# Optimization experiments

Hardware: AMD Instinct MI355X
Metric: run time of the kernel (lower is better)

## Reference

```python
import jax, jax.numpy as jnp
import numpy as np
import math

T_SCALE = 99
FEAT_DIM = 400
BATCH = 2
C = 256
NH = 8
NS = 32
NSPB = 3
RATIO = 0.5
LOCAL_STEP = 33


def build_sample_mask(T=T_SCALE, ns=NS, nspb=NSPB, ratio=RATIO):
    # Vectorized port of _get_interp1d_mask. Flat layout: [time, (bin, start, end)].
    N = ns * nspb
    e_idx, s_idx = np.meshgrid(np.arange(T), np.arange(T), indexing='ij')
    valid = s_idx < e_idx
    starts_i = s_idx[valid].astype(np.int64)
    ends_i = e_idx[valid].astype(np.int64)
    starts = starts_i.astype(np.float64)
    ends = ends_i.astype(np.float64)
    center = ends - starts + 1.0
    xmin = starts - center * ratio
    plen = (ends + center * ratio) - xmin
    S = xmin[:, None] + (plen / (N - 1.0))[:, None] * np.arange(N)[None, :]  # [P, N]
    down = np.trunc(S).astype(np.int64)  # matches int(math.modf(s)[1]) (trunc toward 0)
    dec = S - down                       # can be negative when s < 0, as in the original
    up = np.ceil(S).astype(np.int64)
    bin_col = (np.arange(N) // nspb)[None, :] * (T * T) + (starts_i * T + ends_i)[:, None]
    M = np.zeros(T * ns * T * T, np.float64)
    vd = (down >= 0) & (down <= T - 1)
    np.add.at(M, (down * (ns * T * T) + bin_col)[vd], ((1.0 - dec) / nspb)[vd])
    vu = (up >= 0) & (up <= T - 1)
    np.add.at(M, (up * (ns * T * T) + bin_col)[vu], (dec / nspb)[vu])
    return M.reshape(T, ns * T * T).astype(np.float32)


def pos_ebb(scale, size):
    pos = jnp.arange(scale, dtype=jnp.float32)[:, None]
    div = jnp.exp(jnp.arange(0, size, 2, dtype=jnp.float32) * (-math.log(10000.0) / size))
    ang = pos * div
    # interleave sin (even) / cos (odd)
    return jnp.stack([jnp.sin(ang), jnp.cos(ang)], axis=-1).reshape(scale, size)


def layer_norm(x, g, b, eps=1e-5):
    mu = jnp.mean(x, -1, keepdims=True)
    var = jnp.mean((x - mu) ** 2, -1, keepdims=True)
    return (x - mu) * jax.lax.rsqrt(var + eps) * g + b


def mha(x, w_qkv, b_qkv, w_o, b_o, nh=NH):
    t, b, c = x.shape
    hd = c // nh
    q, k, v = jnp.split(x @ w_qkv.T + b_qkv, 3, axis=-1)
    q = q.reshape(t, b, nh, hd)
    k = k.reshape(t, b, nh, hd)
    v = v.reshape(t, b, nh, hd)
    att = jnp.einsum('qbhd,kbhd->bhqk', q, k) / math.sqrt(hd)
    att = jax.nn.softmax(att, axis=-1)
    o = jnp.einsum('bhqk,kbhd->qbhd', att, v).reshape(t, b, c)
    return o @ w_o.T + b_o


def encoder(x, p):
    # PyTorch post-norm TransformerEncoder (eval mode, dropout off) + final LayerNorm
    (qkv_w, qkv_b, o_w, o_b, l1_w, l1_b, l2_w, l2_b, n1_g, n1_b, n2_g, n2_b, nf_g, nf_b) = p
    for i in range(qkv_w.shape[0]):
        a = mha(x, qkv_w[i], qkv_b[i], o_w[i], o_b[i])
        x = layer_norm(x + a, n1_g[i], n1_b[i])
        f = jax.nn.relu(x @ l1_w[i].T + l1_b[i]) @ l2_w[i].T + l2_b[i]
        x = layer_norm(x + f, n2_g[i], n2_b[i])
    return layer_norm(x, nf_g, nf_b)


def conv1d(x, w, b, pad, groups=1):
    y = jax.lax.conv_general_dilated(x, w, (1,), [(pad, pad)],
                                     dimension_numbers=('NCH', 'OIH', 'NCH'),
                                     feature_group_count=groups)
    return y + b[None, :, None]


def conv2d(x, w, b, pad):
    y = jax.lax.conv_general_dilated(x, w, (1, 1), [(pad, pad), (pad, pad)],
                                     dimension_numbers=('NCHW', 'OIHW', 'NCHW'))
    return y + b[None, :, None, None]


def conv3d(x, w, b, stride):
    y = jax.lax.conv_general_dilated(x, w, stride, [(0, 0)] * 3,
                                     dimension_numbers=('NCDHW', 'OIDHW', 'NCDHW'))
    return y + b[None, :, None, None, None]


def _forward(x, cb_w, cb_b, tg_qkv_w, tg_qkv_b, tg_o_w, tg_o_b, tg_l1_w, tg_l1_b, tg_l2_w, tg_l2_b, tg_n1_g, tg_n1_b, tg_n2_g, tg_n2_b, tg_nf_g, tg_nf_b, tl_qkv_w, tl_qkv_b, tl_o_w, tl_o_b, tl_l1_w, tl_l1_b, tl_l2_w, tl_l2_b, tl_n1_g, tl_n1_b, tl_n2_g, tl_n2_b, tl_nf_g, tl_nf_b, s1_w, s1_b, s2_w, s2_b, c3_w, c3_b, p1_w, p1_b, p2_w, p2_b, p3_w, p3_b, sample_mask):
    B, _, T = x.shape
    base = jax.nn.relu(conv1d(x, cb_w, cb_b, pad=1, groups=4))  # [B,C,T]
    # local transformer on LOCAL_STEP-strided windows
    group = T // LOCAL_STEP
    tl_p = (tl_qkv_w, tl_qkv_b, tl_o_w, tl_o_b, tl_l1_w, tl_l1_b, tl_l2_w, tl_l2_b, tl_n1_g, tl_n1_b, tl_n2_g, tl_n2_b, tl_nf_g, tl_nf_b)
    feat = base.reshape(B, C, LOCAL_STEP, group).transpose(2, 3, 0, 1).reshape(LOCAL_STEP, B * group, C)
    feat = encoder(feat + pos_ebb(LOCAL_STEP, C)[:, None, :], tl_p)
    local = feat.reshape(LOCAL_STEP * group, B, C).transpose(1, 2, 0)  # [B,C,T]
    # global bidirectional transformer (shared weights, flipped second pass)
    tg_p = (tg_qkv_w, tg_qkv_b, tg_o_w, tg_o_b, tg_l1_w, tg_l1_b, tg_l2_w, tg_l2_b, tg_n1_g, tg_n1_b, tg_n2_g, tg_n2_b, tg_nf_g, tg_nf_b)
    g = base.transpose(2, 0, 1)  # [T,B,C]
    pe = pos_ebb(T, C)[:, None, :]
    f1 = encoder(g + pe, tg_p)
    f2 = encoder(g[::-1] + pe, tg_p)
    base2 = local + (f1 + f2[::-1]).transpose(1, 2, 0)  # [B,C,T]
    s = jax.nn.relu(conv1d(base2, s1_w, s1_b, pad=1, groups=4))
    start1 = jax.nn.sigmoid(conv1d(s, s2_w, s2_b, pad=0))[:, 0, :]  # [B,T]
    # boundary-matching layer: dense matmul against precomputed interp mask
    bm = jnp.matmul(base2, sample_mask).reshape(B, C, NS, T, T)
    p = jax.nn.relu(conv3d(bm, c3_w, c3_b, (NS, 1, 1)))[:, :, 0]  # [B,C,T,T]
    p = jax.nn.relu(conv2d(p, p1_w, p1_b, pad=1))
    p = jax.nn.relu(conv2d(p, p2_w, p2_b, pad=1))
    cm = jax.nn.sigmoid(conv2d(p, p3_w, p3_b, pad=0))  # [B,2,T,T]
    return cm, start1


def setup_inputs() -> dict:
    key = jax.random.key(0)
    ks = iter(jax.random.split(key, 80))
    def rnd(shape):
        return 0.02 * jax.random.normal(next(ks), shape, dtype=jnp.float32)
    inp = {'x': jax.random.normal(next(ks), (BATCH, FEAT_DIM, T_SCALE), dtype=jnp.float32)}
    inp['cb_w'] = rnd((C, FEAT_DIM // 4, 3)); inp['cb_b'] = jnp.zeros((C,), jnp.float32)
    for pre, n in (('tg', 6), ('tl', 3)):
        inp[pre + '_qkv_w'] = rnd((n, 3 * C, C)); inp[pre + '_qkv_b'] = jnp.zeros((n, 3 * C), jnp.float32)
        inp[pre + '_o_w'] = rnd((n, C, C)); inp[pre + '_o_b'] = jnp.zeros((n, C), jnp.float32)
        inp[pre + '_l1_w'] = rnd((n, 1024, C)); inp[pre + '_l1_b'] = jnp.zeros((n, 1024), jnp.float32)
        inp[pre + '_l2_w'] = rnd((n, C, 1024)); inp[pre + '_l2_b'] = jnp.zeros((n, C), jnp.float32)
        inp[pre + '_n1_g'] = jnp.ones((n, C), jnp.float32); inp[pre + '_n1_b'] = jnp.zeros((n, C), jnp.float32)
        inp[pre + '_n2_g'] = jnp.ones((n, C), jnp.float32); inp[pre + '_n2_b'] = jnp.zeros((n, C), jnp.float32)
        inp[pre + '_nf_g'] = jnp.ones((C,), jnp.float32); inp[pre + '_nf_b'] = jnp.zeros((C,), jnp.float32)
    inp['s1_w'] = rnd((C, C // 4, 3)); inp['s1_b'] = jnp.zeros((C,), jnp.float32)
    inp['s2_w'] = rnd((1, C, 1)); inp['s2_b'] = jnp.zeros((1,), jnp.float32)
    inp['c3_w'] = rnd((C, C, NS, 1, 1)); inp['c3_b'] = jnp.zeros((C,), jnp.float32)
    inp['p1_w'] = rnd((C, C, 3, 3)); inp['p1_b'] = jnp.zeros((C,), jnp.float32)
    inp['p2_w'] = rnd((C, C, 3, 3)); inp['p2_b'] = jnp.zeros((C,), jnp.float32)
    inp['p3_w'] = rnd((2, C, 1, 1)); inp['p3_b'] = jnp.zeros((2,), jnp.float32)
    inp['sample_mask'] = jnp.asarray(build_sample_mask())  # [T, NS*T*T], exact BMN interp mask
    return inp


def reference(x, cb_w, cb_b, tg_qkv_w, tg_qkv_b, tg_o_w, tg_o_b, tg_l1_w, tg_l1_b, tg_l2_w, tg_l2_b, tg_n1_g, tg_n1_b, tg_n2_g, tg_n2_b, tg_nf_g, tg_nf_b, tl_qkv_w, tl_qkv_b, tl_o_w, tl_o_b, tl_l1_w, tl_l1_b, tl_l2_w, tl_l2_b, tl_n1_g, tl_n1_b, tl_n2_g, tl_n2_b, tl_nf_g, tl_nf_b, s1_w, s1_b, s2_w, s2_b, c3_w, c3_b, p1_w, p1_b, p2_w, p2_b, p3_w, p3_b, sample_mask):
    return _forward(x, cb_w, cb_b, tg_qkv_w, tg_qkv_b, tg_o_w, tg_o_b, tg_l1_w, tg_l1_b, tg_l2_w, tg_l2_b, tg_n1_g, tg_n1_b, tg_n2_g, tg_n2_b, tg_nf_g, tg_nf_b, tl_qkv_w, tl_qkv_b, tl_o_w, tl_o_b, tl_l1_w, tl_l1_b, tl_l2_w, tl_l2_b, tl_n1_g, tl_n1_b, tl_n2_g, tl_n2_b, tl_nf_g, tl_nf_b, s1_w, s1_b, s2_w, s2_b, c3_w, c3_b, p1_w, p1_b, p2_w, p2_b, p3_w, p3_b, sample_mask)
```

## Files before the change

kernel.cpp:

```cpp
#include <hip/hip_runtime.h>
#include <math.h>

#define T99   99
#define CC    256
#define NHH   8
#define FEAT  400
#define NS_   32
#define LSTEP 33

typedef __attribute__((ext_vector_type(8))) short s8v;
typedef __attribute__((ext_vector_type(4))) float f4v;

__device__ __forceinline__ void mfma_bf16(f4v& d, s8v a, s8v b) {
  asm volatile("v_mfma_f32_16x16x32_bf16 %0, %1, %2, %0" : "+v"(d) : "v"(a), "v"(b));
}

__device__ __forceinline__ unsigned short f2bf(float f) {
  union { float f; unsigned u; } x; x.f = f;
  unsigned r = x.u + 0x7FFFu + ((x.u >> 16) & 1u);
  return (unsigned short)(r >> 16);
}
__device__ __forceinline__ float bf2f(unsigned short h) {
  union { unsigned u; float f; } x; x.u = ((unsigned)h) << 16;
  return x.f;
}
__device__ __forceinline__ float blo(unsigned u) { union { unsigned x; float f; } c; c.x = u << 16; return c.f; }
__device__ __forceinline__ float bhi(unsigned u) { union { unsigned x; float f; } c; c.x = u & 0xffff0000u; return c.f; }

__device__ __forceinline__ float pe_val(int pos, int c) {
  int i = c >> 1;
  float freq = expf((float)(2 * i) * (-0.03597789207803197f));
  float ang = (float)pos * freq;
  return (c & 1) ? cosf(ang) : sinf(ang);
}

__global__ __launch_bounds__(128) void k_convbase(const float* __restrict__ x,
                                                  const float* __restrict__ w,
                                                  const float* __restrict__ bias,
                                                  float* __restrict__ base) {
  int b = blockIdx.x >> 8, co = blockIdx.x & 255, t = threadIdx.x;
  if (t >= T99) return;
  int g = co >> 6;
  float acc = bias[co];
  const float* xp = x + (size_t)(b * FEAT + g * 100) * T99;
  const float* wp = w + (size_t)co * 300;
  for (int ic = 0; ic < 100; ++ic) {
    float x0 = (t > 0)  ? xp[ic * T99 + t - 1] : 0.f;
    float x1 = xp[ic * T99 + t];
    float x2 = (t < 98) ? xp[ic * T99 + t + 1] : 0.f;
    acc += wp[ic * 3] * x0 + wp[ic * 3 + 1] * x1 + wp[ic * 3 + 2] * x2;
  }
  base[(size_t)(b * CC + co) * T99 + t] = fmaxf(acc, 0.f);
}

__global__ __launch_bounds__(256) void k_convW(const float* __restrict__ qkv, const float* __restrict__ o,
                                               const float* __restrict__ l1, const float* __restrict__ l2,
                                               int L, unsigned short* __restrict__ dst) {
  int total = L * 786432;
  for (int idx = blockIdx.x * 256 + threadIdx.x; idx < total; idx += gridDim.x * 256) {
    int l = idx / 786432, r = idx % 786432;
    float v;
    if (r < 196608)      v = qkv[(size_t)l * 196608 + r];
    else if (r < 262144) v = o[(size_t)l * 65536 + (r - 196608)];
    else if (r < 524288) v = l1[(size_t)l * 262144 + (r - 262144)];
    else                 v = l2[(size_t)l * 262144 + (r - 524288)];
    dst[idx] = f2bf(v);
  }
}

__global__ __launch_bounds__(256) void k_build_xg(const float* __restrict__ base, float* __restrict__ xg,
                                                  unsigned short* __restrict__ xgb) {
  int idx = blockIdx.x * 256 + threadIdx.x;
  int t = idx >> 10, r = idx & 1023, b4 = r >> 8, c = r & 255;
  float v = (b4 < 2) ? base[(size_t)(b4 * CC + c) * T99 + t]
                     : base[(size_t)((b4 - 2) * CC + c) * T99 + (98 - t)];
  v += pe_val(t, c);
  xg[idx] = v; xgb[idx] = f2bf(v);
}

__global__ __launch_bounds__(256) void k_build_xl(const float* __restrict__ base, float* __restrict__ xl,
                                                  unsigned short* __restrict__ xlb) {
  int idx = blockIdx.x * 256 + threadIdx.x;
  int ls = idx / 1536, r = idx % 1536, j = r >> 8, c = r & 255;
  int g = j >> 1, b = j & 1, t = ls * 3 + g;
  float v = base[(size_t)(b * CC + c) * T99 + t] + pe_val(ls, c);
  xl[idx] = v; xlb[idx] = f2bf(v);
}

__device__ __forceinline__ void gemm_body(const unsigned short* __restrict__ A,
                                          const unsigned short* __restrict__ W,
                                          const float* __restrict__ bias,
                                          const float* __restrict__ R,
                                          float* __restrict__ Y,
                                          unsigned short* __restrict__ Yb,
                                          int M, int N, int K, int flags,
                                          int m0, int n0) {
  __shared__ __align__(16) unsigned short Al[64][40];
  __shared__ __align__(16) unsigned short Bl[64][40];
  int tid = threadIdx.x;
  int lane = tid & 63, w = tid >> 6, wm = w >> 1, wn = w & 1;
  int sp = tid >> 2, kc = (tid & 3) << 3;
  f4v zero4 = {0.f, 0.f, 0.f, 0.f};
  f4v acc[2][2];
#pragma unroll
  for (int mt = 0; mt < 2; ++mt)
#pragma unroll
    for (int nt = 0; nt < 2; ++nt) acc[mt][nt] = zero4;

  for (int k0 = 0; k0 < K; k0 += 32) {
    s8v av = {0, 0, 0, 0, 0, 0, 0, 0};
    int row = m0 + sp;
    if (row < M) av = *(const s8v*)&A[(size_t)row * K + k0 + kc];
    *(s8v*)&Al[sp][kc] = av;
    *(s8v*)&Bl[sp][kc] = *(const s8v*)&W[(size_t)(n0 + sp) * K + k0 + kc];
    __syncthreads();
    s8v af[2], bf[2];
#pragma unroll
    for (int mt = 0; mt < 2; ++mt)
      af[mt] = *(const s8v*)&Al[wm * 32 + mt * 16 + (lane & 15)][(lane >> 4) * 8];
#pragma unroll
    for (int nt = 0; nt < 2; ++nt)
      bf[nt] = *(const s8v*)&Bl[wn * 32 + nt * 16 + (lane & 15)][(lane >> 4) * 8];
#pragma unroll
    for (int mt = 0; mt < 2; ++mt)
#pragma unroll
      for (int nt = 0; nt < 2; ++nt) mfma_bf16(acc[mt][nt], af[mt], bf[nt]);
    __syncthreads();
  }
  asm volatile("s_nop 7\n\ts_nop 7\n\ts_nop 4");
#pragma unroll
  for (int mt = 0; mt < 2; ++mt) {
#pragma unroll
    for (int nt = 0; nt < 2; ++nt) {
      int col = n0 + wn * 32 + nt * 16 + (lane & 15);
      float bv = bias[col];
#pragma unroll
      for (int r = 0; r < 2 * 2; ++r) {
        int row = m0 + wm * 32 + mt * 16 + (lane >> 4) * 4 + r;
        if (row < M) {
          float v = acc[mt][nt][r] + bv;
          if (flags & 2) v += R[(size_t)row * N + col];
          if (flags & 1) v = fmaxf(v, 0.f);
          if (!(flags & 8)) Y[(size_t)row * N + col] = v;
          if (flags & 4) Yb[(size_t)row * N + col] = f2bf(v);
        }
      }
    }
  }
}

__global__ __launch_bounds__(256) void k_gemmb(const unsigned short* __restrict__ A,
                                               const unsigned short* __restrict__ W,
                                               const float* __restrict__ bias,
                                               const float* __restrict__ R,
                                               float* __restrict__ Y,
                                               unsigned short* __restrict__ Yb,
                                               int M, int N, int K, int flags) {
  gemm_body(A, W, bias, R, Y, Yb, M, N, K, flags, blockIdx.x * 64, blockIdx.y * 64);
}

__global__ __launch_bounds__(256) void k_gemmb2(const unsigned short* __restrict__ A0,
                                                const unsigned short* __restrict__ W0,
                                                const float* __restrict__ bias0,
                                                const float* __restrict__ R0,
                                                float* __restrict__ Y0,
                                                unsigned short* __restrict__ Yb0,
                                                int M0,
                                                const unsigned short* __restrict__ A1,
                                                const unsigned short* __restrict__ W1,
                                                const float* __restrict__ bias1,
                                                const float* __restrict__ R1,
                                                float* __restrict__ Y1,
                                                unsigned short* __restrict__ Yb1,
                                                int M1,
                                                int N, int K, int flags) {
  int m0 = blockIdx.x * 64;
  if (blockIdx.z == 0) {
    if (m0 >= M0) return;
    gemm_body(A0, W0, bias0, R0, Y0, Yb0, M0, N, K, flags, m0, blockIdx.y * 64);
  } else {
    if (m0 >= M1) return;
    gemm_body(A1, W1, bias1, R1, Y1, Yb1, M1, N, K, flags, m0, blockIdx.y * 64);
  }
}

__device__ __forceinline__ void attn_body(const unsigned short* __restrict__ qkv,
                                          unsigned short* __restrict__ attb,
                                          int T_, int B_, int bid) {
  __shared__ float qv[32];
  __shared__ float red[128];
  __shared__ float pv[128];
  int tid = threadIdx.x;
  int q = bid % T_;
  int h = (bid / T_) % NHH;
  int b = bid / (T_ * NHH);
  if (tid < 32) qv[tid] = bf2f(qkv[(size_t)(q * B_ + b) * 768 + h * 32 + tid]);
  __syncthreads();
  float s = -1e30f;
  if (tid < T_) {
    const unsigned short* kp = qkv + (size_t)(tid * B_ + b) * 768 + 256 + h * 32;
    float d = 0;
#pragma unroll
    for (int i = 0; i < 32; ++i) d += qv[i] * bf2f(kp[i]);
    s = d * 0.176776695296636881f;
  }
  red[tid] = s; __syncthreads();
  for (int o = 64; o > 0; o >>= 1) { if (tid < o) red[tid] = fmaxf(red[tid], red[tid + o]); __syncthreads(); }
  float mx = red[0]; __syncthreads();
  float p = (tid < T_) ? expf(s - mx) : 0.f;
  pv[tid] = p; red[tid] = p; __syncthreads();
  for (int o = 64; o > 0; o >>= 1) { if (tid < o) red[tid] += red[tid + o]; __syncthreads(); }
  float denom = red[0];
  if (tid < 32) {
    float o = 0;
    for (int k = 0; k < T_; ++k) o += pv[k] * bf2f(qkv[(size_t)(k * B_ + b) * 768 + 512 + h * 32 + tid]);
    attb[(size_t)(q * B_ + b) * 256 + h * 32 + tid] = f2bf(o / denom);
  }
}

__global__ __launch_bounds__(128) void k_attn(const unsigned short* __restrict__ qkv,
                                              unsigned short* __restrict__ attb,
                                              int T_, int B_) {
  attn_body(qkv, attb, T_, B_, blockIdx.x);
}

__global__ __launch_bounds__(128) void k_attn2(const unsigned short* __restrict__ qkv0,
                                               unsigned short* __restrict__ attb0, int T0, int B0,
                                               const unsigned short* __restrict__ qkv1,
                                               unsigned short* __restrict__ attb1, int T1, int B1) {
  int bid = blockIdx.x;
  if (blockIdx.z == 0) {
    if (bid >= B0 * NHH * T0) return;
    attn_body(qkv0, attb0, T0, B0, bid);
  } else {
    if (bid >= B1 * NHH * T1) return;
    attn_body(qkv1, attb1, T1, B1, bid);
  }
}

__device__ __forceinline__ void ln_body(const float* __restrict__ X, const float* __restrict__ g,
                                        const float* __restrict__ bb, float* __restrict__ Y,
                                        unsigned short* __restrict__ Yb, int tok) {
  __shared__ float rs[256], rq[256];
  int c = threadIdx.x;
  float v = X[(size_t)tok * 256 + c];
  rs[c] = v; rq[c] = v * v; __syncthreads();
  for (int o = 128; o > 0; o >>= 1) { if (c < o) { rs[c] += rs[c + o]; rq[c] += rq[c + o]; } __syncthreads(); }
  float mu = rs[0] * (1.f / 256.f);
  float var = rq[0] * (1.f / 256.f) - mu * mu;
  float r = (v - mu) * rsqrtf(var + 1e-5f) * g[c] + bb[c];
  Y[(size_t)tok * 256 + c] = r;
  if (Yb) Yb[(size_t)tok * 256 + c] = f2bf(r);
}

__global__ __launch_bounds__(256) void k_ln(const float* __restrict__ X, const float* __restrict__ g,
                                            const float* __restrict__ bb, float* __restrict__ Y,
                                            unsigned short* __restrict__ Yb) {
  ln_body(X, g, bb, Y, Yb, blockIdx.x);
}

__global__ __launch_bounds__(256) void k_ln2(const float* __restrict__ X0, const float* __restrict__ g0,
                                             const float* __restrict__ bb0, float* __restrict__ Y0,
                                             unsigned short* __restrict__ Yb0, int n0,
                                             const float* __restrict__ X1, const float* __restrict__ g1,
                                             const float* __restrict__ bb1, float* __restrict__ Y1,
                                             unsigned short* __restrict__ Yb1, int n1) {
  int tok = blockIdx.x;
  if (blockIdx.z == 0) {
    if (tok >= n0) return;
    ln_body(X0, g0, bb0, Y0, Yb0, tok);
  } else {
    if (tok >= n1) return;
    ln_body(X1, g1, bb1, Y1, Yb1, tok);
  }
}

__global__ __launch_bounds__(256) void k_combine(const float* __restrict__ encl, const float* __restrict__ encg,
                                                 float* __restrict__ base2) {
  int idx = blockIdx.x * 256 + threadIdx.x;
  int t = idx % T99, c = (idx / T99) & 255, b = idx / (CC * T99);
  int ls = t / 3, g = t % 3;
  float v = encl[(size_t)(ls * 6 + g * 2 + b) * 256 + c]
          + encg[(size_t)(t * 4 + b) * 256 + c]
          + encg[(size_t)((98 - t) * 4 + 2 + b) * 256 + c];
  base2[idx] = v;
}

__global__ __launch_bounds__(128) void k_s1(const float* __restrict__ base2, const float* __restrict__ w,
                                            const float* __restrict__ bias, float* __restrict__ sbuf) {
  int b = blockIdx.x >> 8, co = blockIdx.x & 255, t = threadIdx.x;
  if (t >= T99) return;
  int g = co >> 6;
  float acc = bias[co];
  const float* xp = base2 + (size_t)(b * CC + g * 64) * T99;
  const float* wp = w + (size_t)co * 192;
  for (int ic = 0; ic < 64; ++ic) {
    float x0 = (t > 0)  ? xp[ic * T99 + t - 1] : 0.f;
    float x1 = xp[ic * T99 + t];
    float x2 = (t < 98) ? xp[ic * T99 + t + 1] : 0.f;
    acc += wp[ic * 3] * x0 + wp[ic * 3 + 1] * x1 + wp[ic * 3 + 2] * x2;
  }
  sbuf[(size_t)(b * CC + co) * T99 + t] = fmaxf(acc, 0.f);
}

__global__ __launch_bounds__(256) void k_s2(const float* __restrict__ sbuf, const float* __restrict__ w,
                                            const float* __restrict__ bias, float* __restrict__ out) {
  __shared__ float rs[256];
  int b = blockIdx.x / T99, t = blockIdx.x % T99, c = threadIdx.x;
  rs[c] = w[c] * sbuf[(size_t)(b * CC + c) * T99 + t];
  __syncthreads();
  for (int o = 128; o > 0; o >>= 1) { if (c < o) rs[c] += rs[c + o]; __syncthreads(); }
  if (c == 0) out[blockIdx.x] = 1.f / (1.f + expf(-(rs[0] + bias[0])));
}

__global__ __launch_bounds__(256) void k_w3t(const float* __restrict__ c3w, float* __restrict__ w3t) {
  int idx = blockIdx.x * 256 + threadIdx.x;
  int co = idx & 255, ci = (idx >> 8) & 255, n = idx >> 16;
  w3t[idx] = c3w[((size_t)(co << 8) + ci) * 32 + n];
}

__global__ __launch_bounds__(256) void k_G(const float* __restrict__ w3t, const float* __restrict__ base2,
                                           unsigned short* __restrict__ Gb) {
  int tc = blockIdx.x, n = blockIdx.y, b = blockIdx.z;
  int co = threadIdx.x;
  int t0 = tc * 25;
  float acc[25];
#pragma unroll
  for (int q = 0; q < 25; ++q) acc[q] = 0.f;
  const float* w = w3t + (size_t)n * 65536 + co;
  const float* bs = base2 + (size_t)b * CC * T99 + t0;
  for (int ci = 0; ci < 256; ++ci) {
    float wv = w[(size_t)ci * 256];
#pragma unroll
    for (int q = 0; q < 25; ++q) acc[q] += wv * bs[ci * T99 + q];
  }
#pragma unroll
  for (int q = 0; q < 25; ++q) {
    int t = t0 + q;
    if (t < T99) Gb[((size_t)(n * T99 + t) * 256 + co) * 2 + b] = f2bf(acc[q]);
  }
  if (tc == 0 && n == 0 && b == 0)
    ((unsigned int*)(Gb + (size_t)NS_ * T99 * 512))[co] = 0u;
}

__global__ __launch_bounds__(128) void k_ppre(const unsigned short* __restrict__ Gb,
                                              const float* __restrict__ c3b,
                                              unsigned int* __restrict__ pinb32) {
  __shared__ float w0s[96], w1s[96];
  __shared__ int   ofs[96];
  int e = blockIdx.x % T99, s = blockIdx.x / T99;
  int tid = threadIdx.x;
  if (s >= e) {
    float z0 = fmaxf(c3b[2 * tid], 0.f), z1 = fmaxf(c3b[2 * tid + 1], 0.f);
    unsigned int zz = ((unsigned)f2bf(z1) << 16) | (unsigned)f2bf(z0);
    pinb32[((size_t)(0 * T99 + s) * T99 + e) * 128 + tid] = zz;
    pinb32[((size_t)(1 * T99 + s) * T99 + e) * 128 + tid] = zz;
    return;
  }
  if (tid < 96) {
    double center = (double)(e - s + 1);
    double S = ((double)s - 0.5 * center) + ((2.0 * center - 1.0) / 95.0) * (double)tid;
    double dn = trunc(S);
    double dec = S - dn;
    int di = (int)dn;
    double uc = ceil(S);
    int ui = (int)uc;
    int n = tid / 3;
    float w0 = 0.f, w1 = 0.f;
    int r0 = 0;
    if (dn >= 0.0 && dn <= 98.0) {
      r0 = di;
      w0 = (float)((1.0 - dec) / 3.0);
      if (uc >= 0.0 && uc <= 98.0) {
        if (ui == di) w0 += (float)(dec / 3.0);
        else          w1  = (float)(dec / 3.0);
      }
    }
    w0s[tid] = w0; w1s[tid] = w1;
    ofs[tid] = (n * T99 + r0) * 1024;
  }
  __syncthreads();
  float a00 = 0.f, a01 = 0.f, a10 = 0.f, a11 = 0.f;
  const char* basep = (const char*)Gb + tid * 8;
#pragma unroll 8
  for (int k = 0; k < 96; ++k) {
    float w0 = w0s[k], w1 = w1s[k];
    const uint2* p = (const uint2*)(basep + ofs[k]);
    uint2 u0 = p[0];
    uint2 u1 = p[128];
    a00 += w0 * blo(u0.x) + w1 * blo(u1.x);
    a01 += w0 * bhi(u0.x) + w1 * bhi(u1.x);
    a10 += w0 * blo(u0.y) + w1 * blo(u1.y);
    a11 += w0 * bhi(u0.y) + w1 * bhi(u1.y);
  }
  float b0 = c3b[2 * tid], b1 = c3b[2 * tid + 1];
  unsigned int zb0 = ((unsigned)f2bf(fmaxf(a10 + b1, 0.f)) << 16) | (unsigned)f2bf(fmaxf(a00 + b0, 0.f));
  unsigned int zb1 = ((unsigned)f2bf(fmaxf(a11 + b1, 0.f)) << 16) | (unsigned)f2bf(fmaxf(a01 + b0, 0.f));
  pinb32[((size_t)(0 * T99 + s) * T99 + e) * 128 + tid] = zb0;
  pinb32[((size_t)(1 * T99 + s) * T99 + e) * 128 + tid] = zb1;
}

__global__ __launch_bounds__(256) void k_wb2(const float* __restrict__ pw, unsigned short* __restrict__ wbf) {
  int idx = blockIdx.x * 256 + threadIdx.x;
  if (idx >= 73728) return;
  int lane = idx & 63;
  int cog  = (idx >> 6) & 15;
  int kst  = (idx >> 10) & 7;
  int tap  = idx >> 13;
  int co = cog * 16 + (lane & 15);
  int k  = kst * 32 + (lane >> 4) * 8;
  s8v v;
#pragma unroll
  for (int j = 0; j < 8; ++j)
    v[j] = (short)f2bf(pw[((size_t)co * 256 + k + j) * 9 + tap]);
  *(s8v*)&wbf[(size_t)idx * 8] = v;
}

__global__ __launch_bounds__(256) void k_conv3x3(const unsigned short* __restrict__ in,
                                                 const unsigned short* __restrict__ wbf,
                                                 const float* __restrict__ bias,
                                                 unsigned short* __restrict__ out) {
  __shared__ __align__(16) unsigned short Ah[100 * 264];
  int b = blockIdx.z;
  int co0 = blockIdx.y * 128;
  int ti = blockIdx.x / 13, tj = blockIdx.x % 13;
  int i0 = ti * 8, j0 = tj * 8;
  int tid = threadIdx.x;
#pragma unroll
  for (int it = 0; it < 13; ++it) {
    int chunk = it * 256 + tid;
    if (chunk < 3200) {
      int row = chunk >> 5;
      int cc = (chunk & 31) * 8;
      int gi = i0 + row / 10 - 1, gj = j0 + row % 10 - 1;
      s8v val = {0, 0, 0, 0, 0, 0, 0, 0};
      if (gi >= 0 && gi < T99 && gj >= 0 && gj < T99)
        val = *(const s8v*)&in[((size_t)(b * T99 + gi) * T99 + gj) * 256 + cc];
      *(s8v*)&Ah[row * 264 + cc] = val;
    }
  }
  __syncthreads();

  int lane = tid & 63, w = tid >> 6, wm = w >> 1, wn = w & 1;
  int l15 = lane & 15, lk = lane >> 4;
  int spL0 = wm * 32 + l15;
  int spL1 = spL0 + 16;
  int hr0 = (spL0 >> 3) * 10 + (spL0 & 7) + 11;
  int hr1 = (spL1 >> 3) * 10 + (spL1 & 7) + 11;
  int cogbase = blockIdx.y * 8 + wn * 4;

  f4v acc[2][4];
#pragma unroll
  for (int mt = 0; mt < 2; ++mt)
#pragma unroll
    for (int nt = 0; nt < 4; ++nt) acc[mt][nt] = (f4v){0.f, 0.f, 0.f, 0.f};

  for (int tap = 0; tap < 9; ++tap) {
    int doff = (tap / 3) * 10 + (tap % 3) - 11;
    const unsigned short* bbase = wbf + ((size_t)(tap * 8) * 16) * 512 + (size_t)lane * 8;
#pragma unroll
    for (int kst = 0; kst < 8; ++kst) {
      int k0 = kst * 32;
      s8v a0 = *(const s8v*)&Ah[(hr0 + doff) * 264 + k0 + lk * 8];
      s8v a1 = *(const s8v*)&Ah[(hr1 + doff) * 264 + k0 + lk * 8];
      const unsigned short* bp = bbase + ((size_t)(kst * 16 + cogbase)) * 512;
#pragma unroll
      for (int nt = 0; nt < 4; ++nt) {
        s8v bf = *(const s8v*)&bp[(size_t)nt * 512];
        mfma_bf16(acc[0][nt], a0, bf);
        mfma_bf16(acc[1][nt], a1, bf);
      }
    }
  }
  asm volatile("s_nop 7\n\ts_nop 7\n\ts_nop 4");
#pragma unroll
  for (int mt = 0; mt < 2; ++mt) {
#pragma unroll
    for (int nt = 0; nt < 4; ++nt) {
      int co = co0 + wn * 64 + nt * 16 + l15;
      float bv = bias[co];
#pragma unroll
      for (int r = 0; r < 4; ++r) {
        int sp = wm * 32 + mt * 16 + lk * 4 + r;
        int gi = i0 + (sp >> 3), gj = j0 + (sp & 7);
        if (gi < T99 && gj < T99) {
          float v = fmaxf(acc[mt][nt][r] + bv, 0.f);
          out[((size_t)(b * T99 + gi) * T99 + gj) * 256 + co] = f2bf(v);
        }
      }
    }
  }
}

__global__ __launch_bounds__(256) void k_p3(const unsigned short* __restrict__ p2o,
                                            const float* __restrict__ w, const float* __restrict__ bias,
                                            float* __restrict__ cm) {
  int idx = blockIdx.x * 256 + threadIdx.x;
  if (idx >= 2 * 2 * T99 * T99) return;
  int j = idx % T99, i = (idx / T99) % T99, c2 = (idx / (T99 * T99)) % 2, b = idx / (2 * T99 * T99);
  float acc = bias[c2];
  const unsigned short* row = p2o + ((size_t)(b * T99 + i) * T99 + j) * 256;
  const float* wr = w + c2 * 256;
  for (int c8 = 0; c8 < 256; c8 += 8) {
    s8v v = *(const s8v*)&row[c8];
#pragma unroll
    for (int q = 0; q < 8; ++q) acc += wr[c8 + q] * bf2f((unsigned short)v[q]);
  }
  cm[idx] = 1.f / (1.f + expf(-acc));
}

struct EncW {
  const float *qkvw, *qkvb, *ow, *ob, *l1w, *l1b, *l2w, *l2b, *n1g, *n1b, *n2g, *n2b, *nfg, *nfb;
};

static void enc_layer(float* X, unsigned short* Xb, int ntok, int l,
                      const EncW& W, const unsigned short* Wb,
                      unsigned short* qkvbb, unsigned short* attb, float* yb,
                      int T_, int B_, hipStream_t st) {
  int mg = (ntok + 63) / 64;
  const unsigned short* wq = Wb + (size_t)l * 786432;
  k_gemmb<<<dim3(mg, 12), dim3(256), 0, st>>>(Xb, wq, W.qkvb + l * 768, nullptr, nullptr, qkvbb,
                                              ntok, 768, 256, 4 | 8);
  k_attn<<<dim3(B_ * NHH * T_), dim3(128), 0, st>>>(qkvbb, attb, T_, B_);
  k_gemmb<<<dim3(mg, 4), dim3(256), 0, st>>>(attb, wq + 196608, W.ob + l * 256, X, yb, nullptr,
                                             ntok, 256, 256, 2);
  k_ln<<<dim3(ntok), dim3(256), 0, st>>>(yb, W.n1g + l * 256, W.n1b + l * 256, X, Xb);
  k_gemmb<<<dim3(mg, 16), dim3(256), 0, st>>>(Xb, wq + 262144, W.l1b + l * 1024, nullptr, nullptr, qkvbb,
                                              ntok, 1024, 256, 1 | 4 | 8);
  k_gemmb<<<dim3(mg, 4), dim3(256), 0, st>>>(qkvbb, wq + 524288, W.l2b + l * 256, X, yb, nullptr,
                                             ntok, 256, 1024, 2);
  k_ln<<<dim3(ntok), dim3(256), 0, st>>>(yb, W.n2g + l * 256, W.n2b + l * 256, X, Xb);
}

extern "C" void kernel_launch(void* const* d_in, const int* in_sizes, int n_in,
                              void* d_out, int out_size, void* d_ws, size_t ws_size,
                              hipStream_t stream) {
  (void)in_sizes; (void)n_in; (void)out_size; (void)ws_size;
  const float* x    = (const float*)d_in[0];
  const float* cbw  = (const float*)d_in[1];
  const float* cbb  = (const float*)d_in[2];
  EncW tg = {(const float*)d_in[3],  (const float*)d_in[4],  (const float*)d_in[5],  (const float*)d_in[6],
             (const float*)d_in[7],  (const float*)d_in[8],  (const float*)d_in[9],  (const float*)d_in[10],
             (const float*)d_in[11], (const float*)d_in[12], (const float*)d_in[13], (const float*)d_in[14],
             (const float*)d_in[15], (const float*)d_in[16]};
  EncW tl = {(const float*)d_in[17], (const float*)d_in[18], (const float*)d_in[19], (const float*)d_in[20],
             (const float*)d_in[21], (const float*)d_in[22], (const float*)d_in[23], (const float*)d_in[24],
             (const float*)d_in[25], (const float*)d_in[26], (const float*)d_in[27], (const float*)d_in[28],
             (const float*)d_in[29], (const float*)d_in[30]};
  const float* s1w = (const float*)d_in[31];
  const float* s1b = (const float*)d_in[32];
  const float* s2w = (const float*)d_in[33];
  const float* s2b = (const float*)d_in[34];
  const float* c3w = (const float*)d_in[35];
  const float* c3b = (const float*)d_in[36];
  const float* p1w = (const float*)d_in[37];
  const float* p1b = (const float*)d_in[38];
  const float* p2w = (const float*)d_in[39];
  const float* p2b = (const float*)d_in[40];
  const float* p3w = (const float*)d_in[41];
  const float* p3b = (const float*)d_in[42];

  float* outp = (float*)d_out;

  char* wp = (char*)d_ws;
  auto alloc = [&](size_t bytes) -> void* {
    void* p = (void*)wp;
    wp += (bytes + 255) & ~(size_t)255;
    return p;
  };
  float* base  = (float*)alloc(sizeof(float) * 2 * CC * T99);
  float* xg    = (float*)alloc(sizeof(float) * T99 * 4 * CC);
  float* xl    = (float*)alloc(sizeof(float) * LSTEP * 6 * CC);
  unsigned short* xgb = (unsigned short*)alloc(sizeof(short) * T99 * 4 * CC);
  unsigned short* xlb = (unsigned short*)alloc(sizeof(short) * LSTEP * 6 * CC);
  unsigned short* qkvbbG = (unsigned short*)alloc(sizeof(short) * 396 * 1024);
  unsigned short* qkvbbL = (unsigned short*)alloc(sizeof(short) * 198 * 1024);
  unsigned short* attbG  = (unsigned short*)alloc(sizeof(short) * 396 * 256);
  unsigned short* attbL  = (unsigned short*)alloc(sizeof(short) * 198 * 256);
  float* ybG   = (float*)alloc(sizeof(float) * 396 * 256);
  float* ybL   = (float*)alloc(sizeof(float) * 198 * 256);
  float* encg  = (float*)alloc(sizeof(float) * T99 * 4 * CC);
  float* encl  = (float*)alloc(sizeof(float) * LSTEP * 6 * CC);
  float* base2 = (float*)alloc(sizeof(float) * 2 * CC * T99);
  float* sbuf  = (float*)alloc(sizeof(float) * 2 * CC * T99);
  float* w3t   = (float*)alloc(sizeof(float) * 32 * 256 * 256);
  unsigned short* Gb = (unsigned short*)alloc(sizeof(short) * (2 * NS_ * T99 * 256 + 512));
  unsigned short* pinb = (unsigned short*)alloc(sizeof(short) * 2 * T99 * T99 * 256);
  unsigned short* p1o  = (unsigned short*)alloc(sizeof(short) * 2 * T99 * T99 * 256);
  unsigned short* p2o  = (unsigned short*)alloc(sizeof(short) * 2 * T99 * T99 * 256);
  unsigned short* wb2a = (unsigned short*)alloc(sizeof(short) * 9 * 256 * 256);
  unsigned short* wb2b = (unsigned short*)alloc(sizeof(short) * 9 * 256 * 256);
  unsigned short* wtgb = (unsigned short*)alloc(sizeof(short) * 6 * 786432);
  unsigned short* wtlb = (unsigned short*)alloc(sizeof(short) * 3 * 786432);

  k_convW<<<dim3(4096), dim3(256), 0, stream>>>(tg.qkvw, tg.ow, tg.l1w, tg.l2w, 6, wtgb);
  k_convW<<<dim3(2048), dim3(256), 0, stream>>>(tl.qkvw, tl.ow, tl.l1w, tl.l2w, 3, wtlb);
  k_w3t<<<dim3(8192), dim3(256), 0, stream>>>(c3w, w3t);
  k_wb2<<<dim3(288), dim3(256), 0, stream>>>(p1w, wb2a);
  k_wb2<<<dim3(288), dim3(256), 0, stream>>>(p2w, wb2b);
  k_convbase<<<dim3(512), dim3(128), 0, stream>>>(x, cbw, cbb, base);
  k_build_xl<<<dim3(198), dim3(256), 0, stream>>>(base, xl, xlb);
  k_build_xg<<<dim3(396), dim3(256), 0, stream>>>(base, xg, xgb);

  const int ML = 198, MG = 396;
  const int mgG = 7;
  for (int l = 0; l < 3; ++l) {
    const unsigned short* wqL = wtlb + (size_t)l * 786432;
    const unsigned short* wqG = wtgb + (size_t)l * 786432;
    k_gemmb2<<<dim3(mgG, 12, 2), dim3(256), 0, stream>>>(
        xlb, wqL, tl.qkvb + l * 768, nullptr, nullptr, qkvbbL, ML,
        xgb, wqG, tg.qkvb + l * 768, nullptr, nullptr, qkvbbG, MG, 768, 256, 4 | 8);
    k_attn2<<<dim3(4 * NHH * T99, 1, 2), dim3(128), 0, stream>>>(
        qkvbbL, attbL, LSTEP, 6, qkvbbG, attbG, T99, 4);
    k_gemmb2<<<dim3(mgG, 4, 2), dim3(256), 0, stream>>>(
        attbL, wqL + 196608, tl.ob + l * 256, xl, ybL, nullptr, ML,
        attbG, wqG + 196608, tg.ob + l * 256, xg, ybG, nullptr, MG, 256, 256, 2);
    k_ln2<<<dim3(MG, 1, 2), dim3(256), 0, stream>>>(
        ybL, tl.n1g + l * 256, tl.n1b + l * 256, xl, xlb, ML,
        ybG, tg.n1g + l * 256, tg.n1b + l * 256, xg, xgb, MG);
    k_gemmb2<<<dim3(mgG, 16, 2), dim3(256), 0, stream>>>(
        xlb, wqL + 262144, tl.l1b + l * 1024, nullptr, nullptr, qkvbbL, ML,
        xgb, wqG + 262144, tg.l1b + l * 1024, nullptr, nullptr, qkvbbG, MG, 1024, 256, 1 | 4 | 8);
    k_gemmb2<<<dim3(mgG, 4, 2), dim3(256), 0, stream>>>(
        qkvbbL, wqL + 524288, tl.l2b + l * 256, xl, ybL, nullptr, ML,
        qkvbbG, wqG + 524288, tg.l2b + l * 256, xg, ybG, nullptr, MG, 256, 1024, 2);
    k_ln2<<<dim3(MG, 1, 2), dim3(256), 0, stream>>>(
        ybL, tl.n2g + l * 256, tl.n2b + l * 256, xl, xlb, ML,
        ybG, tg.n2g + l * 256, tg.n2b + l * 256, xg, xgb, MG);
  }
  for (int l = 3; l < 6; ++l)
    enc_layer(xg, xgb, MG, l, tg, wtgb, qkvbbG, attbG, ybG, T99, 4, stream);
  k_ln2<<<dim3(MG, 1, 2), dim3(256), 0, stream>>>(
      xl, tl.nfg, tl.nfb, encl, nullptr, ML,
      xg, tg.nfg, tg.nfb, encg, nullptr, MG);
  k_combine<<<dim3(198), dim3(256), 0, stream>>>(encl, encg, base2);
  k_s1<<<dim3(512), dim3(128), 0, stream>>>(base2, s1w, s1b, sbuf);
  k_s2<<<dim3(198), dim3(256), 0, stream>>>(sbuf, s2w, s2b, outp + 2 * 2 * T99 * T99);
  k_G<<<dim3(4, 32, 2), dim3(256), 0, stream>>>(w3t, base2, Gb);
  k_ppre<<<dim3(T99 * T99), dim3(128), 0, stream>>>(Gb, c3b, (unsigned int*)pinb);
  k_conv3x3<<<dim3(169, 2, 2), dim3(256), 0, stream>>>(pinb, wb2a, p1b, p1o);
  k_conv3x3<<<dim3(169, 2, 2), dim3(256), 0, stream>>>(p1o, wb2b, p2b, p2o);
  k_p3<<<dim3(154), dim3(256), 0, stream>>>(p2o, p3w, p3b, outp);
}
```

Measured before the change: 759.6 us.

## Skip constant lower-triangle conv tiles and software-pipeline conv3x3 MFMA loads

Where the start index is at or past the end index, the proposal-map input to the 3x3 convs is a constant vector derived from the c3 bias. A small kernel precomputes each conv's output for that constant input, and tiles whose halo lies entirely in that region write the vector directly instead of running the MFMA loop. The MFMA main loop is also flattened into 72 steps that prefetch B three stages ahead and A one step ahead, and the asm volatile qualifier is dropped so the compiler can schedule the instructions. The shortcut depends on the triangular zero structure of the interpolation mask and on correct halo bounds, with a different region offset for the second conv.

```diff
diff --git a/kernel.cpp b/kernel.cpp
--- a/kernel.cpp
+++ b/kernel.cpp
@@ -12,7 +12,7 @@
 typedef __attribute__((ext_vector_type(4))) float f4v;
 
 __device__ __forceinline__ void mfma_bf16(f4v& d, s8v a, s8v b) {
-  asm volatile("v_mfma_f32_16x16x32_bf16 %0, %1, %2, %0" : "+v"(d) : "v"(a), "v"(b));
+  asm("v_mfma_f32_16x16x32_bf16 %0, %1, %2, %0" : "+v"(d) : "v"(a), "v"(b));
 }
 
 __device__ __forceinline__ unsigned short f2bf(float f) {
@@ -416,9 +416,41 @@
   *(s8v*)&wbf[(size_t)idx * 8] = v;
 }
 
+__global__ __launch_bounds__(256) void k_cvec(const float* __restrict__ pw, const float* __restrict__ cin,
+                                              const float* __restrict__ bias, int reluCin,
+                                              float* __restrict__ coutF, unsigned short* __restrict__ coutB) {
+  __shared__ float rs[256];
+  int co = blockIdx.x, ci = threadIdx.x;
+  float c = cin[ci];
+  if (reluCin) c = fmaxf(c, 0.f);
+  const float* wp = pw + ((size_t)co * 256 + ci) * 9;
+  float wsum = 0.f;
+#pragma unroll
+  for (int t = 0; t < 9; ++t) wsum += wp[t];
+  rs[ci] = wsum * c;
+  __syncthreads();
+  for (int o = 128; o > 0; o >>= 1) { if (ci < o) rs[ci] += rs[ci + o]; __syncthreads(); }
+  if (ci == 0) {
+    float r = fmaxf(bias[co] + rs[0], 0.f);
+    coutF[co] = r;
+    coutB[co] = f2bf(r);
+  }
+}
+
+__device__ __forceinline__ int aoff(int s) {
+  int tap = s >> 3, kst = s & 7;
+  return ((tap / 3) * 10 + (tap % 3)) * 264 + kst * 32;
+}
+__device__ __forceinline__ void ldb4(const unsigned short* __restrict__ B0, int s, s8v* dst) {
+#pragma unroll
+  for (int nt = 0; nt < 4; ++nt) dst[nt] = *(const s8v*)(B0 + (size_t)s * 8192 + nt * 512);
+}
+
 __global__ __launch_bounds__(256) void k_conv3x3(const unsigned short* __restrict__ in,
                                                  const unsigned short* __restrict__ wbf,
                                                  const float* __restrict__ bias,
+                                                 const unsigned short* __restrict__ cvecB,
+                                                 int D, int lo, int hi,
                                                  unsigned short* __restrict__ out) {
   __shared__ __align__(16) unsigned short Ah[100 * 264];
   int b = blockIdx.z;
@@ -426,6 +458,20 @@
   int ti = blockIdx.x / 13, tj = blockIdx.x % 13;
   int i0 = ti * 8, j0 = tj * 8;
   int tid = threadIdx.x;
+
+  if (i0 - 1 >= lo && i0 + 8 <= hi && j0 - 1 >= lo && j0 + 8 <= hi && i0 - 1 >= j0 + 8 + D) {
+    const unsigned int* cv = (const unsigned int*)(cvecB + co0);
+    unsigned int* ob = (unsigned int*)out;
+#pragma unroll
+    for (int r = 0; r < 16; ++r) {
+      int idx = r * 256 + tid;
+      int sp = idx >> 6, cp = idx & 63;
+      int gi = i0 + (sp >> 3), gj = j0 + (sp & 7);
+      ob[((size_t)(b * T99 + gi) * T99 + gj) * 128 + (co0 >> 1) + cp] = cv[cp];
+    }
+    return;
+  }
+
 #pragma unroll
   for (int it = 0; it < 13; ++it) {
     int chunk = it * 256 + tid;
@@ -443,11 +489,13 @@
 
   int lane = tid & 63, w = tid >> 6, wm = w >> 1, wn = w & 1;
   int l15 = lane & 15, lk = lane >> 4;
-  int spL0 = wm * 32 + l15;
-  int spL1 = spL0 + 16;
-  int hr0 = (spL0 >> 3) * 10 + (spL0 & 7) + 11;
-  int hr1 = (spL1 >> 3) * 10 + (spL1 & 7) + 11;
+  int spL0 = wm * 32 + l15, spL1 = spL0 + 16;
+  int hr0 = (spL0 >> 3) * 10 + (spL0 & 7);
+  int hr1 = (spL1 >> 3) * 10 + (spL1 & 7);
+  const unsigned short* A0 = &Ah[hr0 * 264 + lk * 8];
+  const unsigned short* A1 = &Ah[hr1 * 264 + lk * 8];
   int cogbase = blockIdx.y * 8 + wn * 4;
+  const unsigned short* B0 = wbf + (size_t)cogbase * 512 + (size_t)lane * 8;
 
   f4v acc[2][4];
 #pragma unroll
@@ -455,23 +503,28 @@
 #pragma unroll
     for (int nt = 0; nt < 4; ++nt) acc[mt][nt] = (f4v){0.f, 0.f, 0.f, 0.f};
 
-  for (int tap = 0; tap < 9; ++tap) {
-    int doff = (tap / 3) * 10 + (tap % 3) - 11;
-    const unsigned short* bbase = wbf + ((size_t)(tap * 8) * 16) * 512 + (size_t)lane * 8;
-#pragma unroll
-    for (int kst = 0; kst < 8; ++kst) {
-      int k0 = kst * 32;
-      s8v a0 = *(const s8v*)&Ah[(hr0 + doff) * 264 + k0 + lk * 8];
-      s8v a1 = *(const s8v*)&Ah[(hr1 + doff) * 264 + k0 + lk * 8];
-      const unsigned short* bp = bbase + ((size_t)(kst * 16 + cogbase)) * 512;
-#pragma unroll
-      for (int nt = 0; nt < 4; ++nt) {
-        s8v bf = *(const s8v*)&bp[(size_t)nt * 512];
-        mfma_bf16(acc[0][nt], a0, bf);
-        mfma_bf16(acc[1][nt], a1, bf);
-      }
+  s8v a0c, a1c, a0n, a1n;
+  s8v bq[3][4];
+  a0c = *(const s8v*)(A0 + aoff(0));
+  a1c = *(const s8v*)(A1 + aoff(0));
+  a0n = a0c; a1n = a1c;
+  ldb4(B0, 0, bq[0]);
+  ldb4(B0, 1, bq[1]);
+#pragma unroll
+  for (int s = 0; s < 72; ++s) {
+    if (s + 2 < 72) ldb4(B0, s + 2, bq[(s + 2) % 3]);
+    if (s + 1 < 72) {
+      a0n = *(const s8v*)(A0 + aoff(s + 1));
+      a1n = *(const s8v*)(A1 + aoff(s + 1));
     }
-  }
+#pragma unroll
+    for (int nt = 0; nt < 4; ++nt) {
+      mfma_bf16(acc[0][nt], a0c, bq[s % 3][nt]);
+      mfma_bf16(acc[1][nt], a1c, bq[s % 3][nt]);
+    }
+    a0c = a0n; a1c = a1n;
+  }
+
   asm volatile("s_nop 7\n\ts_nop 7\n\ts_nop 4");
 #pragma unroll
   for (int mt = 0; mt < 2; ++mt) {
@@ -592,12 +645,18 @@
   unsigned short* wb2b = (unsigned short*)alloc(sizeof(short) * 9 * 256 * 256);
   unsigned short* wtgb = (unsigned short*)alloc(sizeof(short) * 6 * 786432);
   unsigned short* wtlb = (unsigned short*)alloc(sizeof(short) * 3 * 786432);
+  float* c1F = (float*)alloc(sizeof(float) * 256);
+  unsigned short* c1B = (unsigned short*)alloc(sizeof(short) * 256);
+  float* c2F = (float*)alloc(sizeof(float) * 256);
+  unsigned short* c2B = (unsigned short*)alloc(sizeof(short) * 256);
 
   k_convW<<<dim3(4096), dim3(256), 0, stream>>>(tg.qkvw, tg.ow, tg.l1w, tg.l2w, 6, wtgb);
   k_convW<<<dim3(2048), dim3(256), 0, stream>>>(tl.qkvw, tl.ow, tl.l1w, tl.l2w, 3, wtlb);
   k_w3t<<<dim3(8192), dim3(256), 0, stream>>>(c3w, w3t);
   k_wb2<<<dim3(288), dim3(256), 0, stream>>>(p1w, wb2a);
   k_wb2<<<dim3(288), dim3(256), 0, stream>>>(p2w, wb2b);
+  k_cvec<<<dim3(256), dim3(256), 0, stream>>>(p1w, c3b, p1b, 1, c1F, c1B);
+  k_cvec<<<dim3(256), dim3(256), 0, stream>>>(p2w, c1F, p2b, 0, c2F, c2B);
   k_convbase<<<dim3(512), dim3(128), 0, stream>>>(x, cbw, cbb, base);
   k_build_xl<<<dim3(198), dim3(256), 0, stream>>>(base, xl, xlb);
   k_build_xg<<<dim3(396), dim3(256), 0, stream>>>(base, xg, xgb);
@@ -638,7 +697,7 @@
   k_s2<<<dim3(198), dim3(256), 0, stream>>>(sbuf, s2w, s2b, outp + 2 * 2 * T99 * T99);
   k_G<<<dim3(4, 32, 2), dim3(256), 0, stream>>>(w3t, base2, Gb);
   k_ppre<<<dim3(T99 * T99), dim3(128), 0, stream>>>(Gb, c3b, (unsigned int*)pinb);
-  k_conv3x3<<<dim3(169, 2, 2), dim3(256), 0, stream>>>(pinb, wb2a, p1b, p1o);
-  k_conv3x3<<<dim3(169, 2, 2), dim3(256), 0, stream>>>(p1o, wb2b, p2b, p2o);
+  k_conv3x3<<<dim3(169, 2, 2), dim3(256), 0, stream>>>(pinb, wb2a, p1b, c1B, 0, 0, 98, p1o);
+  k_conv3x3<<<dim3(169, 2, 2), dim3(256), 0, stream>>>(p1o, wb2b, p2b, c2B, 2, 1, 97, p2o);
   k_p3<<<dim3(154), dim3(256), 0, stream>>>(p2o, p3w, p3b, outp);
 }
```

Measured after the change: 675.5 us. 11.1% less time.
